# Optimization experiments

Hardware: AMD Instinct MI355X
Metric: run time of the kernel (lower is better)

Reference implementation:

```python
import jax, jax.numpy as jnp
import numpy as np

B, C, H, W = 32, 256, 56, 56
NUM_ITER = 5

# Row-major upper-triangular (incl. diagonal) flat indices, matching
# torch.ones(C, C).triu().view(-1).nonzero() in the original triuvec.
_r, _c = np.triu_indices(C)
TRIU_IDX = jnp.asarray(_r * C + _c)


def setup_inputs() -> dict:
    key = jax.random.key(0)
    x = jax.random.normal(key, (B, C, H, W), dtype=jnp.float32)
    return {"x": x}


def _cov_pool(x):
    # x: (b, c, h, w) -> sigma = x_n @ ((1/n) I - (1/n^2) J) @ x_n^T : (b, c, c)
    b, c, h, w = x.shape
    n = h * w
    xn = x.reshape(b, c, n)
    s = xn.sum(axis=2)  # (b, c) = x_n @ ones
    gram = jnp.einsum('bcn,bdn->bcd', xn, xn)  # (b, c, c)
    return gram / n - jnp.einsum('bc,bd->bcd', s, s) / (n * n)


def _newton_schulz_sqrt(x, num_iter):
    # x: (b, m, m) SPD; returns approx matrix square root, scaled by sqrt(trace).
    b, m, _ = x.shape
    eye = jnp.eye(m, dtype=x.dtype)
    x_trace = jnp.trace(x, axis1=1, axis2=2)[:, None, None]  # (b, 1, 1)
    a = x / x_trace
    i3 = 3.0 * eye  # broadcasts over batch
    # iteration 0
    b2 = 0.5 * (i3 - a)
    yi = a @ b2
    zi = b2

    def body(carry, _):
        yi, zi = carry
        b2 = 0.5 * (i3 - zi @ yi)
        return (yi @ b2, b2 @ zi), None

    (yi, zi), _ = jax.lax.scan(body, (yi, zi), None, length=num_iter - 1)
    return yi * jnp.sqrt(x_trace)


def _triuvec(x):
    # (b, c, c) -> (b, c*(c+1)//2), row-major upper triangle incl. diagonal
    b, c, _ = x.shape
    return x.reshape(b, c * c)[:, TRIU_IDX]


def reference(x) -> jnp.ndarray:
    cov = _cov_pool(x)
    y = _newton_schulz_sqrt(cov, NUM_ITER)
    return _triuvec(y)
```

## Files before the change

### kernel.cpp

```cpp
#include <hip/hip_runtime.h>
#include <hip/hip_bf16.h>
#include <math.h>

#define BATCH 32
#define C 256
#define HW 3136
#define OUTROW 32896
#define KSPLIT 7
#define KCHUNK 448

typedef __bf16 b8v __attribute__((ext_vector_type(8)));
typedef float  f4v __attribute__((ext_vector_type(4)));

__device__ __forceinline__ unsigned short f2bf(float f) {
    union { float f; unsigned u; } v; v.f = f;
    unsigned r = v.u + 0x7FFFu + ((v.u >> 16) & 1u);
    return (unsigned short)(r >> 16);
}
__device__ __forceinline__ float bf2f(unsigned short h) {
    union { unsigned u; float f; } v; v.u = ((unsigned)h) << 16; return v.f;
}
__device__ __forceinline__ void split2(float x, unsigned short& h, unsigned short& l) {
    h = f2bf(x);
    l = f2bf(x - bf2f(h));
}

__device__ __forceinline__ float wave_sum(float v) {
    for (int o = 32; o; o >>= 1) v += __shfl_down(v, o, 64);
    return v;
}

__global__ void k_prep(const float* __restrict__ x, unsigned short* __restrict__ xh,
                       unsigned short* __restrict__ xl, float* __restrict__ sbuf,
                       float* __restrict__ qbuf) {
    const int row = blockIdx.x;
    const float4* xr = (const float4*)(x + (size_t)row * HW);
    ushort4* hr = (ushort4*)(xh + (size_t)row * HW);
    ushort4* lr = (ushort4*)(xl + (size_t)row * HW);
    float s = 0.f, q = 0.f;
    for (int c = threadIdx.x; c < HW / 4; c += 256) {
        float4 v = xr[c];
        ushort4 h, l;
        split2(v.x, h.x, l.x); split2(v.y, h.y, l.y);
        split2(v.z, h.z, l.z); split2(v.w, h.w, l.w);
        hr[c] = h; lr[c] = l;
        s += v.x + v.y + v.z + v.w;
        q += v.x * v.x + v.y * v.y + v.z * v.z + v.w * v.w;
    }
    s = wave_sum(s); q = wave_sum(q);
    __shared__ float ss[4], qq[4];
    if ((threadIdx.x & 63) == 0) { ss[threadIdx.x >> 6] = s; qq[threadIdx.x >> 6] = q; }
    __syncthreads();
    if (threadIdx.x == 0) {
        sbuf[row] = ss[0] + ss[1] + ss[2] + ss[3];
        qbuf[row] = qq[0] + qq[1] + qq[2] + qq[3];
    }
}

__global__ void k_tr(const float* __restrict__ sbuf, const float* __restrict__ qbuf,
                     float* __restrict__ trbuf, float* __restrict__ strbuf) {
    const int b = blockIdx.x, t = threadIdx.x;
    const float invn = 1.f / (float)HW, invn2 = invn * invn;
    float sv = sbuf[b * C + t];
    float v = qbuf[b * C + t] * invn - sv * sv * invn2;
    v = wave_sum(v);
    __shared__ float red[4];
    if ((t & 63) == 0) red[t >> 6] = v;
    __syncthreads();
    if (t == 0) {
        float tr = red[0] + red[1] + red[2] + red[3];
        trbuf[b] = tr;
        strbuf[b] = sqrtf(tr);
    }
}

__global__ __launch_bounds__(64) void k_gram_split(
    const unsigned short* __restrict__ Xh, const unsigned short* __restrict__ Xl,
    float* __restrict__ part) {
    const int bid = blockIdx.x;
    const int x8 = bid & 7;
    const int t8 = bid >> 3;
    const int pairIdx = t8 % 10;
    const int g = (t8 / 10) * 8 + x8;
    const int b = g & 31;
    const int z = g >> 5;

    int p = pairIdx, tm = 0, rem = 4;
    while (p >= rem) { p -= rem; ++tm; --rem; }
    const int tn = tm + p;

    const int lane = threadIdx.x & 63;
    const int q = lane >> 4, r = lane & 15;
    const size_t mat = (size_t)b * C * (size_t)HW;
    const int kbase = z * KCHUNK + q * 8;

    size_t oA[4], oB[4];
#pragma unroll
    for (int i = 0; i < 4; ++i) {
        oA[i] = mat + (size_t)(tm * 64 + i * 16 + r) * HW + kbase;
        oB[i] = mat + (size_t)(tn * 64 + i * 16 + r) * HW + kbase;
    }

    f4v acc[4][4] = {};
    b8v fAh[2][4], fAl[2][4], fBh[2][4], fBl[2][4];
#define LDG(buf, k0)                                          \
    do {                                                      \
        for (int i = 0; i < 4; ++i) {                         \
            fAh[buf][i] = *(const b8v*)(Xh + oA[i] + (k0));   \
            fAl[buf][i] = *(const b8v*)(Xl + oA[i] + (k0));   \
            fBh[buf][i] = *(const b8v*)(Xh + oB[i] + (k0));   \
            fBl[buf][i] = *(const b8v*)(Xl + oB[i] + (k0));   \
        }                                                     \
    } while (0)

    LDG(0, 0);
#pragma unroll
    for (int kc = 0; kc < KCHUNK / 32; ++kc) {
        const int cb = kc & 1, nb = cb ^ 1;
        if (kc < KCHUNK / 32 - 1) LDG(nb, (kc + 1) * 32);
#pragma unroll
        for (int i = 0; i < 4; ++i)
#pragma unroll
            for (int j = 0; j < 4; ++j) {
                acc[i][j] = __builtin_amdgcn_mfma_f32_16x16x32_bf16(fAh[cb][i], fBh[cb][j], acc[i][j], 0, 0, 0);
                acc[i][j] = __builtin_amdgcn_mfma_f32_16x16x32_bf16(fAh[cb][i], fBl[cb][j], acc[i][j], 0, 0, 0);
                acc[i][j] = __builtin_amdgcn_mfma_f32_16x16x32_bf16(fAl[cb][i], fBh[cb][j], acc[i][j], 0, 0, 0);
            }
    }
#undef LDG

    float* pt = part + (((size_t)pairIdx * BATCH + b) * KSPLIT + z) * 4096;
#pragma unroll
    for (int i = 0; i < 4; ++i)
#pragma unroll
        for (int j = 0; j < 4; ++j)
#pragma unroll
            for (int reg = 0; reg < 4; ++reg) {
                int row = i * 16 + q * 4 + reg;
                int col = j * 16 + r;
                pt[row * 64 + col] = acc[i][j][reg];
            }
}

__global__ __launch_bounds__(256) void k_reduce(
    const float* __restrict__ part, const float* __restrict__ sbuf,
    const float* __restrict__ trbuf,
    unsigned short* __restrict__ Ahh, unsigned short* __restrict__ All,
    unsigned short* __restrict__ Zhh, unsigned short* __restrict__ Zll) {
    const int b = blockIdx.y;
    int p = blockIdx.x, tm = 0, rem = 4;
    while (p >= rem) { p -= rem; ++tm; --rem; }
    const int tn = tm + p;

    const float* pb = part + ((size_t)blockIdx.x * BATCH + b) * KSPLIT * 4096;
    const int t = threadIdx.x;
    const int row = t >> 2, c0 = (t & 3) * 16;

    float s[16];
#pragma unroll
    for (int u = 0; u < 16; ++u) s[u] = 0.f;
    for (int sp = 0; sp < KSPLIT; ++sp) {
        const float* q4 = pb + sp * 4096 + row * 64 + c0;
#pragma unroll
        for (int u4 = 0; u4 < 4; ++u4) {
            float4 v = *(const float4*)(q4 + u4 * 4);
            s[u4 * 4 + 0] += v.x; s[u4 * 4 + 1] += v.y;
            s[u4 * 4 + 2] += v.z; s[u4 * 4 + 3] += v.w;
        }
    }

    const float invn = 1.f / (float)HW, invn2 = invn * invn;
    const float tr = trbuf[b];
    const int gi = tm * 64 + row;
    const float si = sbuf[b * C + gi];
    const size_t mo = (size_t)b * C * C;

    __shared__ unsigned short tAh[64][66], tAl[64][66], tZh[64][66], tZl[64][66];
    unsigned short vAh[16], vAl[16], vZh[16], vZl[16];
#pragma unroll
    for (int u = 0; u < 16; ++u) {
        int gj = tn * 64 + c0 + u;
        float sj = sbuf[b * C + gj];
        float a = (s[u] * invn - si * sj * invn2) / tr;
        split2(a, vAh[u], vAl[u]);
        float zv = ((gi == gj) ? 1.5f : 0.f) - 0.5f * a;
        split2(zv, vZh[u], vZl[u]);
        tAh[row][c0 + u] = vAh[u]; tAl[row][c0 + u] = vAl[u];
        tZh[row][c0 + u] = vZh[u]; tZl[row][c0 + u] = vZl[u];
    }
    size_t off = mo + (size_t)gi * C + tn * 64 + c0;
#pragma unroll
    for (int u4 = 0; u4 < 4; ++u4) {
        *(ushort4*)&Ahh[off + u4 * 4] = *(ushort4*)&vAh[u4 * 4];
        *(ushort4*)&All[off + u4 * 4] = *(ushort4*)&vAl[u4 * 4];
        *(ushort4*)&Zhh[off + u4 * 4] = *(ushort4*)&vZh[u4 * 4];
        *(ushort4*)&Zll[off + u4 * 4] = *(ushort4*)&vZl[u4 * 4];
    }
    if (tm != tn) {
        __syncthreads();
        const int mr = t >> 2, mc0 = (t & 3) * 16;
        size_t moff = mo + (size_t)(tn * 64 + mr) * C + tm * 64 + mc0;
        unsigned short wAh[16], wAl[16], wZh[16], wZl[16];
#pragma unroll
        for (int u = 0; u < 16; ++u) {
            wAh[u] = tAh[mc0 + u][mr]; wAl[u] = tAl[mc0 + u][mr];
            wZh[u] = tZh[mc0 + u][mr]; wZl[u] = tZl[mc0 + u][mr];
        }
#pragma unroll
        for (int u4 = 0; u4 < 4; ++u4) {
            *(ushort4*)&Ahh[moff + u4 * 4] = *(ushort4*)&wAh[u4 * 4];
            *(ushort4*)&All[moff + u4 * 4] = *(ushort4*)&wAl[u4 * 4];
            *(ushort4*)&Zhh[moff + u4 * 4] = *(ushort4*)&wZh[u4 * 4];
            *(ushort4*)&Zll[moff + u4 * 4] = *(ushort4*)&wZl[u4 * 4];
        }
    }
}

__device__ __forceinline__ void wave_gemm64(
    const unsigned short* __restrict__ Ah, const unsigned short* __restrict__ Al,
    const unsigned short* __restrict__ Bh, const unsigned short* __restrict__ Bl,
    int rowA, int rowB, f4v acc[4][4]) {
    const int lane = threadIdx.x & 63;
    const int q = lane >> 4, r = lane & 15;
    size_t oA[4], oB[4];
#pragma unroll
    for (int i = 0; i < 4; ++i) {
        oA[i] = (size_t)(rowA + i * 16 + r) * C + q * 8;
        oB[i] = (size_t)(rowB + i * 16 + r) * C + q * 8;
    }
    b8v fAh[2][4], fAl[2][4], fBh[2][4], fBl[2][4];
#define LD(buf, k0)                                           \
    do {                                                      \
        for (int i = 0; i < 4; ++i) {                         \
            fAh[buf][i] = *(const b8v*)(Ah + oA[i] + (k0));   \
            fAl[buf][i] = *(const b8v*)(Al + oA[i] + (k0));   \
            fBh[buf][i] = *(const b8v*)(Bh + oB[i] + (k0));   \
            fBl[buf][i] = *(const b8v*)(Bl + oB[i] + (k0));   \
        }                                                     \
    } while (0)

    LD(0, 0);
#pragma unroll
    for (int kc = 0; kc < 8; ++kc) {
        const int cb = kc & 1, nb = cb ^ 1;
        if (kc < 7) LD(nb, (kc + 1) * 32);
#pragma unroll
        for (int i = 0; i < 4; ++i)
#pragma unroll
            for (int j = 0; j < 4; ++j) {
                acc[i][j] = __builtin_amdgcn_mfma_f32_16x16x32_bf16(fAh[cb][i], fBh[cb][j], acc[i][j], 0, 0, 0);
                acc[i][j] = __builtin_amdgcn_mfma_f32_16x16x32_bf16(fAh[cb][i], fBl[cb][j], acc[i][j], 0, 0, 0);
                acc[i][j] = __builtin_amdgcn_mfma_f32_16x16x32_bf16(fAl[cb][i], fBh[cb][j], acc[i][j], 0, 0, 0);
            }
    }
#undef LD
}

template <int MODE>
__global__ __launch_bounds__(64) void k_t64(
    const unsigned short* __restrict__ Ah, const unsigned short* __restrict__ Al,
    const unsigned short* __restrict__ Bh, const unsigned short* __restrict__ Bl,
    unsigned short* __restrict__ Dh, unsigned short* __restrict__ Dl,
    float* __restrict__ outF, const float* __restrict__ strbuf) {
    const int bid = blockIdx.x;
    const int x8 = bid & 7;
    const int w = bid >> 3;
    int b, tm, tn;
    if (MODE == 2) {
        b = x8 + 8 * (w / 10);
        int p = w % 10, rem = 4; tm = 0;
        while (p >= rem) { p -= rem; ++tm; --rem; }
        tn = tm + p;
    } else {
        b = x8 + 8 * (w >> 4);
        const int tile = w & 15;
        tm = tile >> 2; tn = tile & 3;
    }
    const size_t mo = (size_t)b * C * C;
    f4v acc[4][4] = {};
    wave_gemm64(Ah + mo, Al + mo, Bh + mo, Bl + mo, tm * 64, tn * 64, acc);

    const int lane = threadIdx.x & 63, q = lane >> 4, r = lane & 15;
    if (MODE == 2) {
        const float sc = strbuf[b];
#pragma unroll
        for (int i = 0; i < 4; ++i)
#pragma unroll
            for (int j = 0; j < 4; ++j) {
                const int gj = tn * 64 + j * 16 + r;
#pragma unroll
                for (int reg = 0; reg < 4; ++reg) {
                    const int gi = tm * 64 + i * 16 + q * 4 + reg;
                    if (gj >= gi)
                        outF[(size_t)b * OUTROW + (size_t)(gi * C - (gi * (gi - 1)) / 2) +
                             (gj - gi)] = acc[i][j][reg] * sc;
                }
            }
    } else {
#pragma unroll
        for (int i = 0; i < 4; ++i)
#pragma unroll
            for (int j = 0; j < 4; ++j) {
                const int gj = tn * 64 + j * 16 + r;
#pragma unroll
                for (int reg = 0; reg < 4; ++reg) {
                    const int gi = tm * 64 + i * 16 + q * 4 + reg;
                    float v = acc[i][j][reg];
                    if (MODE == 1) v = ((gi == gj) ? 1.5f : 0.f) - 0.5f * v;
                    unsigned short h, l;
                    split2(v, h, l);
                    Dh[mo + (size_t)gi * C + gj] = h;
                    Dl[mo + (size_t)gi * C + gj] = l;
                }
            }
    }
}

__global__ __launch_bounds__(64) void k_yz64(
    const unsigned short* __restrict__ Yh, const unsigned short* __restrict__ Yl,
    const unsigned short* __restrict__ Th, const unsigned short* __restrict__ Tl,
    const unsigned short* __restrict__ Zh, const unsigned short* __restrict__ Zl,
    unsigned short* __restrict__ Ynh, unsigned short* __restrict__ Ynl,
    unsigned short* __restrict__ Znh, unsigned short* __restrict__ Znl) {
    const int bid = blockIdx.x;
    const int x8 = bid & 7;
    const int w = bid >> 3;
    const int b = x8 + 8 * ((w >> 4) & 3);
    const int zz = w >> 6;
    const int tile = w & 15;
    const int tm = tile >> 2, tn = tile & 3;

    const unsigned short* Ah = zz ? Th : Yh;
    const unsigned short* Al = zz ? Tl : Yl;
    const unsigned short* Bh = zz ? Zh : Th;
    const unsigned short* Bl = zz ? Zl : Tl;
    unsigned short* Dh = zz ? Znh : Ynh;
    unsigned short* Dl = zz ? Znl : Ynl;

    const size_t mo = (size_t)b * C * C;
    f4v acc[4][4] = {};
    wave_gemm64(Ah + mo, Al + mo, Bh + mo, Bl + mo, tm * 64, tn * 64, acc);

    const int lane = threadIdx.x & 63, q = lane >> 4, r = lane & 15;
#pragma unroll
    for (int i = 0; i < 4; ++i)
#pragma unroll
        for (int j = 0; j < 4; ++j) {
            const int gj = tn * 64 + j * 16 + r;
#pragma unroll
            for (int reg = 0; reg < 4; ++reg) {
                const int gi = tm * 64 + i * 16 + q * 4 + reg;
                unsigned short h, l;
                split2(acc[i][j][reg], h, l);
                Dh[mo + (size_t)gi * C + gj] = h;
                Dl[mo + (size_t)gi * C + gj] = l;
            }
        }
}

extern "C" void kernel_launch(void* const* d_in, const int* in_sizes, int n_in,
                              void* d_out, int out_size, void* d_ws, size_t ws_size,
                              hipStream_t stream) {
    const float* x = (const float*)d_in[0];
    float* out = (float*)d_out;

    unsigned short* W = (unsigned short*)d_ws;
    const size_t XN = (size_t)BATCH * C * HW;
    const size_t M = (size_t)BATCH * C * C;
    unsigned short* XH = W;
    unsigned short* XL = XH + XN;
    float* sbuf = (float*)(XL + XN);
    float* qbuf = sbuf + BATCH * C;
    float* trbuf = qbuf + BATCH * C;
    float* strbuf = trbuf + BATCH;
    unsigned short* P = (unsigned short*)(strbuf + BATCH);
    unsigned short* PA_h = P + 0 * M; unsigned short* PA_l = P + 1 * M;
    unsigned short* PB_h = P + 2 * M; unsigned short* PB_l = P + 3 * M;
    unsigned short* PC_h = P + 4 * M; unsigned short* PC_l = P + 5 * M;
    unsigned short* PD_h = P + 6 * M; unsigned short* PD_l = P + 7 * M;
    unsigned short* PE_h = P + 8 * M; unsigned short* PE_l = P + 9 * M;
    float* part = (float*)PC_h;

    k_prep<<<dim3(BATCH * C), 256, 0, stream>>>(x, XH, XL, sbuf, qbuf);
    k_tr<<<dim3(BATCH), 256, 0, stream>>>(sbuf, qbuf, trbuf, strbuf);
    k_gram_split<<<dim3(10 * BATCH * KSPLIT), 64, 0, stream>>>(XH, XL, part);
    k_reduce<<<dim3(10, BATCH), 256, 0, stream>>>(part, sbuf, trbuf,
                                                  PA_h, PA_l, PB_h, PB_l);

    dim3 g512(512);
    k_t64<0><<<g512, 64, 0, stream>>>(PA_h, PA_l, PB_h, PB_l, PC_h, PC_l, nullptr, strbuf);
    k_t64<1><<<g512, 64, 0, stream>>>(PB_h, PB_l, PC_h, PC_l, PD_h, PD_l, nullptr, strbuf);
    k_yz64<<<dim3(1024), 64, 0, stream>>>(PC_h, PC_l, PD_h, PD_l, PB_h, PB_l,
                                          PA_h, PA_l, PE_h, PE_l);
    k_t64<1><<<g512, 64, 0, stream>>>(PE_h, PE_l, PA_h, PA_l, PB_h, PB_l, nullptr, strbuf);
    k_yz64<<<dim3(1024), 64, 0, stream>>>(PA_h, PA_l, PB_h, PB_l, PE_h, PE_l,
                                          PC_h, PC_l, PD_h, PD_l);
    k_t64<1><<<g512, 64, 0, stream>>>(PD_h, PD_l, PC_h, PC_l, PA_h, PA_l, nullptr, strbuf);
    k_yz64<<<dim3(1024), 64, 0, stream>>>(PC_h, PC_l, PA_h, PA_l, PD_h, PD_l,
                                          PB_h, PB_l, PE_h, PE_l);
    k_t64<1><<<g512, 64, 0, stream>>>(PE_h, PE_l, PB_h, PB_l, PC_h, PC_l, nullptr, strbuf);
    k_t64<2><<<dim3(320), 64, 0, stream>>>(PB_h, PB_l, PC_h, PC_l, nullptr, nullptr,
                                           out, strbuf);
}
```

Baseline: 405.7 us.

## Store bf16 split operands in K-chunked panel layout for contiguous MFMA loads

Changes the intermediate bf16 hi/lo buffers for X and for the Newton-Schulz matrices from row-major to a chunked layout of 32-wide K panels ([chunk][row][32]). Every GEMM load of a 32-column K slice now reads one contiguous 16 KB panel instead of strided rows, which is meant to improve cache-line and TLB locality for the direct global-to-register MFMA fragment loads. Offsets become 32-bit ints. The cost is that the prep kernel and the epilogue stores now scatter across panels, and every producer and consumer must agree on the new layout.

```diff
diff --git a/kernel.cpp b/kernel.cpp
--- a/kernel.cpp
+++ b/kernel.cpp
@@ -8,6 +8,8 @@
 #define OUTROW 32896
 #define KSPLIT 7
 #define KCHUNK 448
+#define KC32 98
+
 
 typedef __bf16 b8v __attribute__((ext_vector_type(8)));
 typedef float  f4v __attribute__((ext_vector_type(4)));
@@ -34,16 +36,19 @@
                        unsigned short* __restrict__ xl, float* __restrict__ sbuf,
                        float* __restrict__ qbuf) {
     const int row = blockIdx.x;
+    const int b = row >> 8, c = row & 255;
     const float4* xr = (const float4*)(x + (size_t)row * HW);
-    ushort4* hr = (ushort4*)(xh + (size_t)row * HW);
-    ushort4* lr = (ushort4*)(xl + (size_t)row * HW);
     float s = 0.f, q = 0.f;
-    for (int c = threadIdx.x; c < HW / 4; c += 256) {
-        float4 v = xr[c];
+    for (int idx = threadIdx.x; idx < HW / 4; idx += 256) {
+        const int k = idx * 4;
+        const int kc = k >> 5, ko = k & 31;
+        float4 v = xr[idx];
         ushort4 h, l;
         split2(v.x, h.x, l.x); split2(v.y, h.y, l.y);
         split2(v.z, h.z, l.z); split2(v.w, h.w, l.w);
-        hr[c] = h; lr[c] = l;
+        const size_t dst = ((size_t)(b * KC32 + kc) * 256 + c) * 32 + ko;
+        *(ushort4*)&xh[dst] = h;
+        *(ushort4*)&xl[dst] = l;
         s += v.x + v.y + v.z + v.w;
         q += v.x * v.x + v.y * v.y + v.z * v.z + v.w * v.w;
     }
@@ -91,33 +96,34 @@
 
     const int lane = threadIdx.x & 63;
     const int q = lane >> 4, r = lane & 15;
-    const size_t mat = (size_t)b * C * (size_t)HW;
-    const int kbase = z * KCHUNK + q * 8;
-
-    size_t oA[4], oB[4];
+    const int kc0 = z * (KCHUNK / 32);
+    const size_t matb = (size_t)b * KC32 * 8192;
+
+    int oA[4], oB[4];
 #pragma unroll
     for (int i = 0; i < 4; ++i) {
-        oA[i] = mat + (size_t)(tm * 64 + i * 16 + r) * HW + kbase;
-        oB[i] = mat + (size_t)(tn * 64 + i * 16 + r) * HW + kbase;
+        oA[i] = (tm * 64 + i * 16 + r) * 32 + q * 8;
+        oB[i] = (tn * 64 + i * 16 + r) * 32 + q * 8;
     }
 
     f4v acc[4][4] = {};
     b8v fAh[2][4], fAl[2][4], fBh[2][4], fBl[2][4];
-#define LDG(buf, k0)                                          \
-    do {                                                      \
-        for (int i = 0; i < 4; ++i) {                         \
-            fAh[buf][i] = *(const b8v*)(Xh + oA[i] + (k0));   \
-            fAl[buf][i] = *(const b8v*)(Xl + oA[i] + (k0));   \
-            fBh[buf][i] = *(const b8v*)(Xh + oB[i] + (k0));   \
-            fBl[buf][i] = *(const b8v*)(Xl + oB[i] + (k0));   \
-        }                                                     \
+#define LDG(buf, kc)                                                     \
+    do {                                                                 \
+        const size_t sb = matb + (size_t)(kc0 + (kc)) * 8192;            \
+        for (int i = 0; i < 4; ++i) {                                    \
+            fAh[buf][i] = *(const b8v*)(Xh + sb + oA[i]);                \
+            fAl[buf][i] = *(const b8v*)(Xl + sb + oA[i]);                \
+            fBh[buf][i] = *(const b8v*)(Xh + sb + oB[i]);                \
+            fBl[buf][i] = *(const b8v*)(Xl + sb + oB[i]);                \
+        }                                                                \
     } while (0)
 
     LDG(0, 0);
 #pragma unroll
     for (int kc = 0; kc < KCHUNK / 32; ++kc) {
         const int cb = kc & 1, nb = cb ^ 1;
-        if (kc < KCHUNK / 32 - 1) LDG(nb, (kc + 1) * 32);
+        if (kc < KCHUNK / 32 - 1) LDG(nb, kc + 1);
 #pragma unroll
         for (int i = 0; i < 4; ++i)
 #pragma unroll
@@ -173,7 +179,7 @@
     const float tr = trbuf[b];
     const int gi = tm * 64 + row;
     const float si = sbuf[b * C + gi];
-    const size_t mo = (size_t)b * C * C;
+    const size_t mb = (size_t)b * 8 * 8192;
 
     __shared__ unsigned short tAh[64][66], tAl[64][66], tZh[64][66], tZl[64][66];
     unsigned short vAh[16], vAl[16], vZh[16], vZl[16];
@@ -188,18 +194,19 @@
         tAh[row][c0 + u] = vAh[u]; tAl[row][c0 + u] = vAl[u];
         tZh[row][c0 + u] = vZh[u]; tZl[row][c0 + u] = vZl[u];
     }
-    size_t off = mo + (size_t)gi * C + tn * 64 + c0;
 #pragma unroll
     for (int u4 = 0; u4 < 4; ++u4) {
-        *(ushort4*)&Ahh[off + u4 * 4] = *(ushort4*)&vAh[u4 * 4];
-        *(ushort4*)&All[off + u4 * 4] = *(ushort4*)&vAl[u4 * 4];
-        *(ushort4*)&Zhh[off + u4 * 4] = *(ushort4*)&vZh[u4 * 4];
-        *(ushort4*)&Zll[off + u4 * 4] = *(ushort4*)&vZl[u4 * 4];
+        const int col0 = tn * 64 + c0 + u4 * 4;
+        const size_t off = mb + (size_t)(col0 >> 5) * 8192 + (size_t)gi * 32 + (col0 & 31);
+        *(ushort4*)&Ahh[off] = *(ushort4*)&vAh[u4 * 4];
+        *(ushort4*)&All[off] = *(ushort4*)&vAl[u4 * 4];
+        *(ushort4*)&Zhh[off] = *(ushort4*)&vZh[u4 * 4];
+        *(ushort4*)&Zll[off] = *(ushort4*)&vZl[u4 * 4];
     }
     if (tm != tn) {
         __syncthreads();
         const int mr = t >> 2, mc0 = (t & 3) * 16;
-        size_t moff = mo + (size_t)(tn * 64 + mr) * C + tm * 64 + mc0;
+        const int gim = tn * 64 + mr;
         unsigned short wAh[16], wAl[16], wZh[16], wZl[16];
 #pragma unroll
         for (int u = 0; u < 16; ++u) {
@@ -208,10 +215,12 @@
         }
 #pragma unroll
         for (int u4 = 0; u4 < 4; ++u4) {
-            *(ushort4*)&Ahh[moff + u4 * 4] = *(ushort4*)&wAh[u4 * 4];
-            *(ushort4*)&All[moff + u4 * 4] = *(ushort4*)&wAl[u4 * 4];
-            *(ushort4*)&Zhh[moff + u4 * 4] = *(ushort4*)&wZh[u4 * 4];
-            *(ushort4*)&Zll[moff + u4 * 4] = *(ushort4*)&wZl[u4 * 4];
+            const int col0 = tm * 64 + mc0 + u4 * 4;
+            const size_t off = mb + (size_t)(col0 >> 5) * 8192 + (size_t)gim * 32 + (col0 & 31);
+            *(ushort4*)&Ahh[off] = *(ushort4*)&wAh[u4 * 4];
+            *(ushort4*)&All[off] = *(ushort4*)&wAl[u4 * 4];
+            *(ushort4*)&Zhh[off] = *(ushort4*)&wZh[u4 * 4];
+            *(ushort4*)&Zll[off] = *(ushort4*)&wZl[u4 * 4];
         }
     }
 }
@@ -222,28 +231,29 @@
     int rowA, int rowB, f4v acc[4][4]) {
     const int lane = threadIdx.x & 63;
     const int q = lane >> 4, r = lane & 15;
-    size_t oA[4], oB[4];
+    int oA[4], oB[4];
 #pragma unroll
     for (int i = 0; i < 4; ++i) {
-        oA[i] = (size_t)(rowA + i * 16 + r) * C + q * 8;
-        oB[i] = (size_t)(rowB + i * 16 + r) * C + q * 8;
+        oA[i] = (rowA + i * 16 + r) * 32 + q * 8;
+        oB[i] = (rowB + i * 16 + r) * 32 + q * 8;
     }
     b8v fAh[2][4], fAl[2][4], fBh[2][4], fBl[2][4];
-#define LD(buf, k0)                                           \
-    do {                                                      \
-        for (int i = 0; i < 4; ++i) {                         \
-            fAh[buf][i] = *(const b8v*)(Ah + oA[i] + (k0));   \
-            fAl[buf][i] = *(const b8v*)(Al + oA[i] + (k0));   \
-            fBh[buf][i] = *(const b8v*)(Bh + oB[i] + (k0));   \
-            fBl[buf][i] = *(const b8v*)(Bl + oB[i] + (k0));   \
-        }                                                     \
+#define LD(buf, kc)                                              \
+    do {                                                         \
+        const size_t sb = (size_t)(kc) * 8192;                   \
+        for (int i = 0; i < 4; ++i) {                            \
+            fAh[buf][i] = *(const b8v*)(Ah + sb + oA[i]);        \
+            fAl[buf][i] = *(const b8v*)(Al + sb + oA[i]);        \
+            fBh[buf][i] = *(const b8v*)(Bh + sb + oB[i]);        \
+            fBl[buf][i] = *(const b8v*)(Bl + sb + oB[i]);        \
+        }                                                        \
     } while (0)
 
     LD(0, 0);
 #pragma unroll
     for (int kc = 0; kc < 8; ++kc) {
         const int cb = kc & 1, nb = cb ^ 1;
-        if (kc < 7) LD(nb, (kc + 1) * 32);
+        if (kc < 7) LD(nb, kc + 1);
 #pragma unroll
         for (int i = 0; i < 4; ++i)
 #pragma unroll
@@ -254,6 +264,29 @@
             }
     }
 #undef LD
+}
+
+__device__ __forceinline__ void store_tile_fm(
+    unsigned short* __restrict__ Dh, unsigned short* __restrict__ Dl,
+    int tm, int tn, const f4v acc[4][4], bool modeT) {
+    const int lane = threadIdx.x & 63, q = lane >> 4, r = lane & 15;
+#pragma unroll
+    for (int i = 0; i < 4; ++i)
+#pragma unroll
+        for (int j = 0; j < 4; ++j) {
+            const int gj = tn * 64 + j * 16 + r;
+            const size_t cbase = (size_t)(gj >> 5) * 8192 + (gj & 31);
+#pragma unroll
+            for (int reg = 0; reg < 4; ++reg) {
+                const int gi = tm * 64 + i * 16 + q * 4 + reg;
+                float v = acc[i][j][reg];
+                if (modeT) v = ((gi == gj) ? 1.5f : 0.f) - 0.5f * v;
+                unsigned short h, l;
+                split2(v, h, l);
+                Dh[cbase + (size_t)gi * 32] = h;
+                Dl[cbase + (size_t)gi * 32] = l;
+            }
+        }
 }
 
 template <int MODE>
@@ -276,12 +309,12 @@
         const int tile = w & 15;
         tm = tile >> 2; tn = tile & 3;
     }
-    const size_t mo = (size_t)b * C * C;
+    const size_t mo = (size_t)b * 8 * 8192;
     f4v acc[4][4] = {};
     wave_gemm64(Ah + mo, Al + mo, Bh + mo, Bl + mo, tm * 64, tn * 64, acc);
 
-    const int lane = threadIdx.x & 63, q = lane >> 4, r = lane & 15;
     if (MODE == 2) {
+        const int lane = threadIdx.x & 63, q = lane >> 4, r = lane & 15;
         const float sc = strbuf[b];
 #pragma unroll
         for (int i = 0; i < 4; ++i)
@@ -297,22 +330,7 @@
                 }
             }
     } else {
-#pragma unroll
-        for (int i = 0; i < 4; ++i)
-#pragma unroll
-            for (int j = 0; j < 4; ++j) {
-                const int gj = tn * 64 + j * 16 + r;
-#pragma unroll
-                for (int reg = 0; reg < 4; ++reg) {
-                    const int gi = tm * 64 + i * 16 + q * 4 + reg;
-                    float v = acc[i][j][reg];
-                    if (MODE == 1) v = ((gi == gj) ? 1.5f : 0.f) - 0.5f * v;
-                    unsigned short h, l;
-                    split2(v, h, l);
-                    Dh[mo + (size_t)gi * C + gj] = h;
-                    Dl[mo + (size_t)gi * C + gj] = l;
-                }
-            }
+        store_tile_fm(Dh + mo, Dl + mo, tm, tn, acc, MODE == 1);
     }
 }
 
@@ -337,25 +355,10 @@
     unsigned short* Dh = zz ? Znh : Ynh;
     unsigned short* Dl = zz ? Znl : Ynl;
 
-    const size_t mo = (size_t)b * C * C;
+    const size_t mo = (size_t)b * 8 * 8192;
     f4v acc[4][4] = {};
     wave_gemm64(Ah + mo, Al + mo, Bh + mo, Bl + mo, tm * 64, tn * 64, acc);
-
-    const int lane = threadIdx.x & 63, q = lane >> 4, r = lane & 15;
-#pragma unroll
-    for (int i = 0; i < 4; ++i)
-#pragma unroll
-        for (int j = 0; j < 4; ++j) {
-            const int gj = tn * 64 + j * 16 + r;
-#pragma unroll
-            for (int reg = 0; reg < 4; ++reg) {
-                const int gi = tm * 64 + i * 16 + q * 4 + reg;
-                unsigned short h, l;
-                split2(acc[i][j][reg], h, l);
-                Dh[mo + (size_t)gi * C + gj] = h;
-                Dl[mo + (size_t)gi * C + gj] = l;
-            }
-        }
+    store_tile_fm(Dh + mo, Dl + mo, tm, tn, acc, false);
 }
 
 extern "C" void kernel_launch(void* const* d_in, const int* in_sizes, int n_in,
```

New measurement: 372.8 us. 1.09x faster.
